# Optimization experiments

Hardware: AMD Instinct MI355X
Metric: run time of the kernel (lower is better)

## Reference

```python
import jax, jax.numpy as jnp
import numpy as np

B, L, HIDDEN, DEPTH, INPUT_DIM = 256, 4096, 128, 2, 2
LOG_PROB_FACTOR = 0.5


def setup_inputs() -> dict:
    key = jax.random.key(0)
    k1, k2, k3, k4 = jax.random.split(key, 4)
    x = jax.random.randint(k1, (B, L), 0, INPUT_DIM)
    # variance-scaling-like init (fan_avg), small scale for recurrent stability
    W_in = jax.random.normal(k2, (INPUT_DIM, HIDDEN), dtype=jnp.float32) * np.float32(
        (2.0 / (INPUT_DIM + HIDDEN)) ** 0.5)
    W_c = jax.random.normal(k3, (DEPTH, HIDDEN, HIDDEN), dtype=jnp.float32) * np.float32(
        (0.1 / HIDDEN) ** 0.5)
    W_out = jax.random.normal(k4, (HIDDEN, INPUT_DIM - 1), dtype=jnp.float32) * np.float32(
        (2.0 / (HIDDEN + INPUT_DIM - 1)) ** 0.5)
    b_out = jnp.zeros((INPUT_DIM - 1,), dtype=jnp.float32)
    return {"x": x, "W_in": W_in, "W_c": W_c, "W_out": W_out, "b_out": b_out}


def reference(x, W_in, W_c, W_out, b_out):
    # x: [B, L] int spins; returns per-sample summed log-prob [B]
    b, l = x.shape
    input_dim = W_in.shape[0]
    depth, hidden = W_c.shape[0], W_c.shape[1]

    oh = jax.nn.one_hot(x, input_dim, dtype=W_in.dtype)       # [B, L, D_in]
    xs = jnp.moveaxis(oh, 1, 0)                                # [L, B, D_in]

    h0 = jnp.zeros((b, depth, hidden), dtype=W_in.dtype)       # zero_carry
    prev0 = jnp.zeros((b, input_dim), dtype=W_in.dtype)        # initial input

    def step(carry, x_t):
        h, prev = carry
        # data_in_dense + actFun (shared across the stack call)
        r = jax.nn.elu(prev @ W_in)                            # [B, H]
        new_h = []
        for j in range(depth):
            # RNNCell: elu(cell_carry_dense(h_j)) + input
            hj = jax.nn.elu(h[:, j] @ W_c[j]) + r              # [B, H]
            new_h.append(hj)
            r = hj
        h_new = jnp.stack(new_h, axis=1)                       # [B, depth, H]
        # output head -> normalized log-probs (realValuedOutput=True)
        logits = r @ W_out + b_out                             # [B, D_in-1]
        amp = jnp.concatenate(
            [jnp.zeros((b, 1), dtype=logits.dtype), logits], axis=-1)  # [B, D_in]
        lp = LOG_PROB_FACTOR * jax.nn.log_softmax(amp, axis=-1)
        log_p = jnp.sum(lp * x_t, axis=-1)                     # [B]
        log_p = jnp.nan_to_num(log_p, nan=-35.0)
        return (h_new, x_t), log_p

    _, log_ps = jax.lax.scan(step, (h0, prev0), xs)            # [L, B]
    return jnp.sum(log_ps, axis=0)                             # [B]
```

## Files before the change

### kernel.cpp

```cpp
#include <hip/hip_runtime.h>
#include <hip/hip_bf16.h>


#define L_LEN 4096
#define HID   128
#define NB    16
#define TPB   512
#define WPITCH 129

typedef float f32x4 __attribute__((ext_vector_type(4)));
typedef short s16x8 __attribute__((ext_vector_type(8)));
typedef short s16x4 __attribute__((ext_vector_type(4)));

__device__ __forceinline__ float eluf(float v) { return v > 0.f ? v : (__expf(v) - 1.f); }
__device__ __forceinline__ unsigned short f2bf(float v) {
    union { __hip_bfloat16 b; unsigned short u; } cv;
    cv.b = __float2bfloat16(v);
    return cv.u;
}
__device__ __forceinline__ float bf2f(unsigned short u) {
    union { float f; unsigned v; } cv;
    cv.v = ((unsigned)u) << 16;
    return cv.f;
}

__global__ __launch_bounds__(TPB, 1)
void rnn_ls_kernel(const int*   __restrict__ x,
                   const float* __restrict__ W_in,
                   const float* __restrict__ W_c,
                   const float* __restrict__ W_out,
                   const float* __restrict__ b_out,
                   float* __restrict__ out)
{
    __shared__ __align__(16) unsigned short hAf[2][2][NB][HID];
    __shared__ unsigned xbsm[NB * WPITCH];
    __shared__ float gbuf[2][4][NB];

    const int T  = threadIdx.x;
    const int w8 = T >> 6;
    const int Lw = w8 >> 2;
    const int wv = w8 & 3;
    const int l  = T & 63, c = l & 15, g = l >> 4;
    const int bb0 = blockIdx.x * NB;
    const int swz = c << 3;

    for (int idx = w8; idx < NB * (L_LEN / 64); idx += 8) {
        int batch = idx >> 6;
        int pos   = ((idx & 63) << 6) + l;
        int v     = x[(bb0 + batch) * L_LEN + pos];
        unsigned long long mask = __ballot(v & 1);
        if (l == 0)  xbsm[batch * WPITCH + ((idx & 63) << 1)]     = (unsigned)mask;
        if (l == 32) xbsm[batch * WPITCH + ((idx & 63) << 1) + 1] = (unsigned)(mask >> 32);
    }
    for (int i = T; i < 2 * 2 * NB * HID; i += TPB) ((unsigned short*)hAf)[i] = 0;

    s16x8 Af[2][4];
    #pragma unroll
    for (int mt = 0; mt < 2; ++mt) {
        const int col = wv * 32 + mt * 16 + c;
        #pragma unroll
        for (int kt = 0; kt < 4; ++kt) {
            s16x8 f;
            #pragma unroll
            for (int j = 0; j < 8; ++j)
                f[j] = (short)f2bf(W_c[(Lw * HID + kt * 32 + g * 8 + j) * HID + col]);
            Af[mt][kt] = f;
        }
    }
    s16x8 woA;
    #pragma unroll
    for (int j = 0; j < 8; ++j)
        woA[j] = (c == 0) ? (short)f2bf(W_out[wv * 32 + g * 8 + j]) : (short)0;

    float R0v[2][4], R1v[2][4];
    #pragma unroll
    for (int mt = 0; mt < 2; ++mt)
      #pragma unroll
      for (int r = 0; r < 4; ++r) {
        int co = wv * 32 + mt * 16 + 4 * g + r;
        R0v[mt][r] = eluf(W_in[co]);
        R1v[mt][r] = eluf(W_in[HID + co]);
      }
    const float b0 = b_out[0];

    const int ro0 = (g * 8) ^ swz,      ro1 = (32 + g * 8) ^ swz;
    const int ro2 = (64 + g * 8) ^ swz, ro3 = (96 + g * 8) ^ swz;
    const int wo0 = (wv * 32 + 4 * g) ^ swz;
    const int wo1 = (wv * 32 + 16 + 4 * g) ^ swz;

    float acc = 0.f;
    unsigned xw = 0;

    __syncthreads();

#define STEP(T_, Q_) do {                                                         \
    const int t_ = (T_);                                                          \
    s16x8 Bv0, Bv1, Bv2, Bv3;                                                     \
    if ((Lw == 1) || (t_ < L_LEN)) {                                              \
        Bv0 = *(const s16x8*)&hAf[Q_][Lw][c][ro0];                                \
        Bv1 = *(const s16x8*)&hAf[Q_][Lw][c][ro1];                                \
        Bv2 = *(const s16x8*)&hAf[Q_][Lw][c][ro2];                                \
        Bv3 = *(const s16x8*)&hAf[Q_][Lw][c][ro3];                                \
    }                                                                             \
    if (Lw == 1) {                   \
        s16x8 Bw = (wv == 0) ? Bv0 : (wv == 1) ? Bv1 : (wv == 2) ? Bv2 : Bv3;     \
        f32x4 Cg = {0.f, 0.f, 0.f, 0.f};                                          \
        Cg = __builtin_amdgcn_mfma_f32_16x16x32_bf16(woA, Bw, Cg, 0, 0, 0);       \
        if (g == 0) gbuf[Q_][wv][c] = Cg[0];                                      \
    }                                                                             \
    if (w8 == 7 && l < 16 && t_ > 1) {                \
        int s_ = t_ - 2;                                                          \
        float gg = gbuf[Q_ ^ 1][0][c] + gbuf[Q_ ^ 1][1][c]                        \
                 + gbuf[Q_ ^ 1][2][c] + gbuf[Q_ ^ 1][3][c] + b0;                  \
        unsigned cw = xbsm[c * WPITCH + (s_ >> 5)];                               \
        int bit = (cw >> (s_ & 31)) & 1;                                          \
        float mm  = fmaxf(gg, 0.f);                                               \
        float lse = mm + __logf(__expf(gg - mm) + __expf(-mm));                   \
        acc += 0.5f * ((bit ? gg : 0.f) - lse);                                   \
    }                                                                             \
    f32x4 CA = {0.f, 0.f, 0.f, 0.f}, CB = {0.f, 0.f, 0.f, 0.f};                   \
    if (t_ < L_LEN) {                                                             \
        CA = __builtin_amdgcn_mfma_f32_16x16x32_bf16(Af[0][0], Bv0, CA, 0, 0, 0); \
        CA = __builtin_amdgcn_mfma_f32_16x16x32_bf16(Af[0][1], Bv1, CA, 0, 0, 0); \
        CA = __builtin_amdgcn_mfma_f32_16x16x32_bf16(Af[0][2], Bv2, CA, 0, 0, 0); \
        CA = __builtin_amdgcn_mfma_f32_16x16x32_bf16(Af[0][3], Bv3, CA, 0, 0, 0); \
        CB = __builtin_amdgcn_mfma_f32_16x16x32_bf16(Af[1][0], Bv0, CB, 0, 0, 0); \
        CB = __builtin_amdgcn_mfma_f32_16x16x32_bf16(Af[1][1], Bv1, CB, 0, 0, 0); \
        CB = __builtin_amdgcn_mfma_f32_16x16x32_bf16(Af[1][2], Bv2, CB, 0, 0, 0); \
        CB = __builtin_amdgcn_mfma_f32_16x16x32_bf16(Af[1][3], Bv3, CB, 0, 0, 0); \
        if (Lw == 0) {                   \
            if (((t_ - 1) & 31) == 0) xw = xbsm[c * WPITCH + ((t_ - 1) >> 5)];    \
            const int bit = (int)((xw >> ((t_ - 1) & 31)) & 1u);                  \
            s16x4 p0, p1;                                                         \
            _Pragma("unroll")                                                     \
            for (int r = 0; r < 4; ++r) {                                         \
                p0[r] = (short)f2bf(eluf(CA[r]) + (bit ? R1v[0][r] : R0v[0][r])); \
                p1[r] = (short)f2bf(eluf(CB[r]) + (bit ? R1v[1][r] : R0v[1][r])); \
            }                                                                     \
            *(s16x4*)&hAf[Q_ ^ 1][0][c][wo0] = p0;                                \
            *(s16x4*)&hAf[Q_ ^ 1][0][c][wo1] = p1;                                \
        }                                                                         \
    }                                                                             \
    __syncthreads();                                                              \
    if (Lw == 1 && t_ < L_LEN) {            \
        s16x4 h0a = *(const s16x4*)&hAf[Q_ ^ 1][0][c][wo0];                       \
        s16x4 h0b = *(const s16x4*)&hAf[Q_ ^ 1][0][c][wo1];                       \
        s16x4 p0, p1;                                                             \
        _Pragma("unroll")                                                         \
        for (int r = 0; r < 4; ++r) {                                             \
            p0[r] = (short)f2bf(eluf(CA[r]) + bf2f((unsigned short)h0a[r]));      \
            p1[r] = (short)f2bf(eluf(CB[r]) + bf2f((unsigned short)h0b[r]));      \
        }                                                                         \
        *(s16x4*)&hAf[Q_ ^ 1][1][c][wo0] = p0;                                    \
        *(s16x4*)&hAf[Q_ ^ 1][1][c][wo1] = p1;                                    \
    }                                                                             \
    __syncthreads();                                                              \
} while (0)

    for (int t = 1; t <= L_LEN; t += 2) {
        STEP(t, 1);
        STEP(t + 1, 0);
    }
#undef STEP

    if (w8 == 7 && l < 16) {
        float gg = gbuf[0][0][c] + gbuf[0][1][c] + gbuf[0][2][c] + gbuf[0][3][c] + b0;
        unsigned cw = xbsm[c * WPITCH + ((L_LEN - 1) >> 5)];
        int bit = (cw >> ((L_LEN - 1) & 31)) & 1;
        float mm  = fmaxf(gg, 0.f);
        float lse = mm + __logf(__expf(gg - mm) + __expf(-mm));
        acc += 0.5f * ((bit ? gg : 0.f) - lse);
        out[bb0 + c] = acc;
    }
}

extern "C" void kernel_launch(void* const* d_in, const int* in_sizes, int n_in,
                              void* d_out, int out_size, void* d_ws, size_t ws_size,
                              hipStream_t stream)
{
    const int*   x     = (const int*)  d_in[0];
    const float* W_in  = (const float*)d_in[1];
    const float* W_c   = (const float*)d_in[2];
    const float* W_out = (const float*)d_in[3];
    const float* b_out = (const float*)d_in[4];
    float* out = (float*)d_out;

    rnn_ls_kernel<<<16, TPB, 0, stream>>>(x, W_in, W_c, W_out, b_out, out);
}
```

Before: 2.756 ms.

## Software-pipeline the two RNN layers across timesteps with one barrier per step

Layer 1 waves now process the previous timestep while layer 0 waves compute the current one, so each step needs a single __syncthreads instead of two. The output-head MFMA and log-softmax are shifted further down the pipeline with a 4-deep gbuf ring, and the loop is extended by extra drain iterations. bf16 packing now uses the v_cvt_pk_bf16_f32 instruction through inline asm. This halves the barrier count on the sequential critical path, in exchange for more complex index bookkeeping and a few extra loop iterations.

```diff
diff --git a/kernel.cpp b/kernel.cpp
--- a/kernel.cpp
+++ b/kernel.cpp
@@ -10,31 +10,32 @@
 
 typedef float f32x4 __attribute__((ext_vector_type(4)));
 typedef short s16x8 __attribute__((ext_vector_type(8)));
-typedef short s16x4 __attribute__((ext_vector_type(4)));
+
+#define MFMA16(A_, B_, C_) __builtin_amdgcn_mfma_f32_16x16x32_bf16((A_), (B_), (C_), 0, 0, 0)
 
 __device__ __forceinline__ float eluf(float v) { return v > 0.f ? v : (__expf(v) - 1.f); }
+__device__ __forceinline__ unsigned cvtpk(float lo, float hi) {
+    unsigned r;
+    asm("v_cvt_pk_bf16_f32 %0, %1, %2" : "=v"(r) : "v"(lo), "v"(hi));
+    return r;
+}
 __device__ __forceinline__ unsigned short f2bf(float v) {
     union { __hip_bfloat16 b; unsigned short u; } cv;
     cv.b = __float2bfloat16(v);
     return cv.u;
 }
-__device__ __forceinline__ float bf2f(unsigned short u) {
-    union { float f; unsigned v; } cv;
-    cv.v = ((unsigned)u) << 16;
-    return cv.f;
-}
 
 __global__ __launch_bounds__(TPB, 1)
-void rnn_ls_kernel(const int*   __restrict__ x,
-                   const float* __restrict__ W_in,
-                   const float* __restrict__ W_c,
-                   const float* __restrict__ W_out,
-                   const float* __restrict__ b_out,
-                   float* __restrict__ out)
+void rnn_pipe_kernel(const int*   __restrict__ x,
+                     const float* __restrict__ W_in,
+                     const float* __restrict__ W_c,
+                     const float* __restrict__ W_out,
+                     const float* __restrict__ b_out,
+                     float* __restrict__ out)
 {
     __shared__ __align__(16) unsigned short hAf[2][2][NB][HID];
     __shared__ unsigned xbsm[NB * WPITCH];
-    __shared__ float gbuf[2][4][NB];
+    __shared__ float gbuf[4][4][NB];
 
     const int T  = threadIdx.x;
     const int w8 = T >> 6;
@@ -85,6 +86,7 @@
 
     const int ro0 = (g * 8) ^ swz,      ro1 = (32 + g * 8) ^ swz;
     const int ro2 = (64 + g * 8) ^ swz, ro3 = (96 + g * 8) ^ swz;
+    const int ro_w = (wv * 32 + g * 8) ^ swz;
     const int wo0 = (wv * 32 + 4 * g) ^ swz;
     const int wo1 = (wv * 32 + 16 + 4 * g) ^ swz;
 
@@ -95,83 +97,93 @@
 
 #define STEP(T_, Q_) do {                                                         \
     const int t_ = (T_);                                                          \
-    s16x8 Bv0, Bv1, Bv2, Bv3;                                                     \
-    if ((Lw == 1) || (t_ < L_LEN)) {                                              \
-        Bv0 = *(const s16x8*)&hAf[Q_][Lw][c][ro0];                                \
-        Bv1 = *(const s16x8*)&hAf[Q_][Lw][c][ro1];                                \
-        Bv2 = *(const s16x8*)&hAf[Q_][Lw][c][ro2];                                \
-        Bv3 = *(const s16x8*)&hAf[Q_][Lw][c][ro3];                                \
-    }                                                                             \
-    if (Lw == 1) {                   \
-        s16x8 Bw = (wv == 0) ? Bv0 : (wv == 1) ? Bv1 : (wv == 2) ? Bv2 : Bv3;     \
-        f32x4 Cg = {0.f, 0.f, 0.f, 0.f};                                          \
-        Cg = __builtin_amdgcn_mfma_f32_16x16x32_bf16(woA, Bw, Cg, 0, 0, 0);       \
-        if (g == 0) gbuf[Q_][wv][c] = Cg[0];                                      \
-    }                                                                             \
-    if (w8 == 7 && l < 16 && t_ > 1) {                \
-        int s_ = t_ - 2;                                                          \
-        float gg = gbuf[Q_ ^ 1][0][c] + gbuf[Q_ ^ 1][1][c]                        \
-                 + gbuf[Q_ ^ 1][2][c] + gbuf[Q_ ^ 1][3][c] + b0;                  \
-        unsigned cw = xbsm[c * WPITCH + (s_ >> 5)];                               \
-        int bit = (cw >> (s_ & 31)) & 1;                                          \
-        float mm  = fmaxf(gg, 0.f);                                               \
-        float lse = mm + __logf(__expf(gg - mm) + __expf(-mm));                   \
-        acc += 0.5f * ((bit ? gg : 0.f) - lse);                                   \
-    }                                                                             \
-    f32x4 CA = {0.f, 0.f, 0.f, 0.f}, CB = {0.f, 0.f, 0.f, 0.f};                   \
-    if (t_ < L_LEN) {                                                             \
-        CA = __builtin_amdgcn_mfma_f32_16x16x32_bf16(Af[0][0], Bv0, CA, 0, 0, 0); \
-        CA = __builtin_amdgcn_mfma_f32_16x16x32_bf16(Af[0][1], Bv1, CA, 0, 0, 0); \
-        CA = __builtin_amdgcn_mfma_f32_16x16x32_bf16(Af[0][2], Bv2, CA, 0, 0, 0); \
-        CA = __builtin_amdgcn_mfma_f32_16x16x32_bf16(Af[0][3], Bv3, CA, 0, 0, 0); \
-        CB = __builtin_amdgcn_mfma_f32_16x16x32_bf16(Af[1][0], Bv0, CB, 0, 0, 0); \
-        CB = __builtin_amdgcn_mfma_f32_16x16x32_bf16(Af[1][1], Bv1, CB, 0, 0, 0); \
-        CB = __builtin_amdgcn_mfma_f32_16x16x32_bf16(Af[1][2], Bv2, CB, 0, 0, 0); \
-        CB = __builtin_amdgcn_mfma_f32_16x16x32_bf16(Af[1][3], Bv3, CB, 0, 0, 0); \
-        if (Lw == 0) {                   \
+    if (Lw == 0) {                                                                \
+        if (t_ < L_LEN) {                                \
+            s16x8 B0 = *(const s16x8*)&hAf[Q_][0][c][ro0];                        \
+            s16x8 B1 = *(const s16x8*)&hAf[Q_][0][c][ro1];                        \
+            s16x8 B2 = *(const s16x8*)&hAf[Q_][0][c][ro2];                        \
+            s16x8 B3 = *(const s16x8*)&hAf[Q_][0][c][ro3];                        \
             if (((t_ - 1) & 31) == 0) xw = xbsm[c * WPITCH + ((t_ - 1) >> 5)];    \
+            f32x4 CA = {0.f,0.f,0.f,0.f}, CB = {0.f,0.f,0.f,0.f};                 \
+            CA = MFMA16(Af[0][0], B0, CA); CA = MFMA16(Af[0][1], B1, CA);         \
+            CA = MFMA16(Af[0][2], B2, CA); CA = MFMA16(Af[0][3], B3, CA);         \
+            CB = MFMA16(Af[1][0], B0, CB); CB = MFMA16(Af[1][1], B1, CB);         \
+            CB = MFMA16(Af[1][2], B2, CB); CB = MFMA16(Af[1][3], B3, CB);         \
             const int bit = (int)((xw >> ((t_ - 1) & 31)) & 1u);                  \
-            s16x4 p0, p1;                                                         \
-            _Pragma("unroll")                                                     \
-            for (int r = 0; r < 4; ++r) {                                         \
-                p0[r] = (short)f2bf(eluf(CA[r]) + (bit ? R1v[0][r] : R0v[0][r])); \
-                p1[r] = (short)f2bf(eluf(CB[r]) + (bit ? R1v[1][r] : R0v[1][r])); \
-            }                                                                     \
-            *(s16x4*)&hAf[Q_ ^ 1][0][c][wo0] = p0;                                \
-            *(s16x4*)&hAf[Q_ ^ 1][0][c][wo1] = p1;                                \
+            float ha0 = eluf(CA[0]) + (bit ? R1v[0][0] : R0v[0][0]);              \
+            float ha1 = eluf(CA[1]) + (bit ? R1v[0][1] : R0v[0][1]);              \
+            float ha2 = eluf(CA[2]) + (bit ? R1v[0][2] : R0v[0][2]);              \
+            float ha3 = eluf(CA[3]) + (bit ? R1v[0][3] : R0v[0][3]);              \
+            float hb0 = eluf(CB[0]) + (bit ? R1v[1][0] : R0v[1][0]);              \
+            float hb1 = eluf(CB[1]) + (bit ? R1v[1][1] : R0v[1][1]);              \
+            float hb2 = eluf(CB[2]) + (bit ? R1v[1][2] : R0v[1][2]);              \
+            float hb3 = eluf(CB[3]) + (bit ? R1v[1][3] : R0v[1][3]);              \
+            uint2 pa, pb;                                                         \
+            pa.x = cvtpk(ha0, ha1); pa.y = cvtpk(ha2, ha3);                       \
+            pb.x = cvtpk(hb0, hb1); pb.y = cvtpk(hb2, hb3);                       \
+            *(uint2*)&hAf[Q_ ^ 1][0][c][wo0] = pa;                                \
+            *(uint2*)&hAf[Q_ ^ 1][0][c][wo1] = pb;                                \
+        }                                                                         \
+    } else {                                                                      \
+        if (t_ >= 2 && t_ <= L_LEN) {                                \
+            s16x8 B0 = *(const s16x8*)&hAf[Q_][1][c][ro0];                        \
+            s16x8 B1 = *(const s16x8*)&hAf[Q_][1][c][ro1];                        \
+            s16x8 B2 = *(const s16x8*)&hAf[Q_][1][c][ro2];                        \
+            s16x8 B3 = *(const s16x8*)&hAf[Q_][1][c][ro3];                        \
+            uint2 a0 = *(const uint2*)&hAf[Q_][0][c][wo0];      \
+            uint2 a1 = *(const uint2*)&hAf[Q_][0][c][wo1];                        \
+            s16x8 Bw = B0;                                                        \
+            if (wv == 1) Bw = B1; else if (wv == 2) Bw = B2;                      \
+            else if (wv == 3) Bw = B3;                                            \
+            f32x4 Cg = {0.f,0.f,0.f,0.f};                                         \
+            Cg = MFMA16(woA, Bw, Cg);          \
+            if (g == 0) gbuf[t_ & 3][wv][c] = Cg[0];                              \
+            f32x4 CA = {0.f,0.f,0.f,0.f}, CB = {0.f,0.f,0.f,0.f};                 \
+            CA = MFMA16(Af[0][0], B0, CA); CA = MFMA16(Af[0][1], B1, CA);         \
+            CA = MFMA16(Af[0][2], B2, CA); CA = MFMA16(Af[0][3], B3, CA);         \
+            CB = MFMA16(Af[1][0], B0, CB); CB = MFMA16(Af[1][1], B1, CB);         \
+            CB = MFMA16(Af[1][2], B2, CB); CB = MFMA16(Af[1][3], B3, CB);         \
+            float ha0 = eluf(CA[0]) + __uint_as_float(a0.x << 16);                \
+            float ha1 = eluf(CA[1]) + __uint_as_float(a0.x & 0xffff0000u);        \
+            float ha2 = eluf(CA[2]) + __uint_as_float(a0.y << 16);                \
+            float ha3 = eluf(CA[3]) + __uint_as_float(a0.y & 0xffff0000u);        \
+            float hb0 = eluf(CB[0]) + __uint_as_float(a1.x << 16);                \
+            float hb1 = eluf(CB[1]) + __uint_as_float(a1.x & 0xffff0000u);        \
+            float hb2 = eluf(CB[2]) + __uint_as_float(a1.y << 16);                \
+            float hb3 = eluf(CB[3]) + __uint_as_float(a1.y & 0xffff0000u);        \
+            uint2 pa, pb;                                                         \
+            pa.x = cvtpk(ha0, ha1); pa.y = cvtpk(ha2, ha3);                       \
+            pb.x = cvtpk(hb0, hb1); pb.y = cvtpk(hb2, hb3);                       \
+            *(uint2*)&hAf[Q_ ^ 1][1][c][wo0] = pa;                                \
+            *(uint2*)&hAf[Q_ ^ 1][1][c][wo1] = pb;                                \
+        } else if (t_ == L_LEN + 1) {                  \
+            s16x8 Bw = *(const s16x8*)&hAf[Q_][1][c][ro_w];                       \
+            f32x4 Cg = {0.f,0.f,0.f,0.f};                                         \
+            Cg = MFMA16(woA, Bw, Cg);                                             \
+            if (g == 0) gbuf[t_ & 3][wv][c] = Cg[0];                              \
+        }                                                                         \
+        if (w8 == 7 && l < 16 && t_ >= 4 && t_ <= L_LEN + 3) {       \
+            int s_ = t_ - 4;                                                      \
+            const float* gp = &gbuf[(t_ - 2) & 3][0][0];                          \
+            float gg = gp[0 * NB + c] + gp[1 * NB + c]                            \
+                     + gp[2 * NB + c] + gp[3 * NB + c] + b0;                      \
+            unsigned cw = xbsm[c * WPITCH + (s_ >> 5)];                           \
+            int bit2 = (cw >> (s_ & 31)) & 1;                                     \
+            float mm  = fmaxf(gg, 0.f);                                           \
+            float lse = mm + __logf(__expf(gg - mm) + __expf(-mm));               \
+            acc += 0.5f * ((bit2 ? gg : 0.f) - lse);                              \
         }                                                                         \
     }                                                                             \
     __syncthreads();                                                              \
-    if (Lw == 1 && t_ < L_LEN) {            \
-        s16x4 h0a = *(const s16x4*)&hAf[Q_ ^ 1][0][c][wo0];                       \
-        s16x4 h0b = *(const s16x4*)&hAf[Q_ ^ 1][0][c][wo1];                       \
-        s16x4 p0, p1;                                                             \
-        _Pragma("unroll")                                                         \
-        for (int r = 0; r < 4; ++r) {                                             \
-            p0[r] = (short)f2bf(eluf(CA[r]) + bf2f((unsigned short)h0a[r]));      \
-            p1[r] = (short)f2bf(eluf(CB[r]) + bf2f((unsigned short)h0b[r]));      \
-        }                                                                         \
-        *(s16x4*)&hAf[Q_ ^ 1][1][c][wo0] = p0;                                    \
-        *(s16x4*)&hAf[Q_ ^ 1][1][c][wo1] = p1;                                    \
-    }                                                                             \
-    __syncthreads();                                                              \
 } while (0)
 
-    for (int t = 1; t <= L_LEN; t += 2) {
+    for (int t = 1; t <= L_LEN + 3; t += 2) {
         STEP(t, 1);
         STEP(t + 1, 0);
     }
 #undef STEP
 
-    if (w8 == 7 && l < 16) {
-        float gg = gbuf[0][0][c] + gbuf[0][1][c] + gbuf[0][2][c] + gbuf[0][3][c] + b0;
-        unsigned cw = xbsm[c * WPITCH + ((L_LEN - 1) >> 5)];
-        int bit = (cw >> ((L_LEN - 1) & 31)) & 1;
-        float mm  = fmaxf(gg, 0.f);
-        float lse = mm + __logf(__expf(gg - mm) + __expf(-mm));
-        acc += 0.5f * ((bit ? gg : 0.f) - lse);
-        out[bb0 + c] = acc;
-    }
+    if (w8 == 7 && l < 16) out[bb0 + c] = acc;
 }
 
 extern "C" void kernel_launch(void* const* d_in, const int* in_sizes, int n_in,
@@ -185,5 +197,5 @@
     const float* b_out = (const float*)d_in[4];
     float* out = (float*)d_out;
 
-    rnn_ls_kernel<<<16, TPB, 0, stream>>>(x, W_in, W_c, W_out, b_out, out);
-}
+    rnn_pipe_kernel<<<16, TPB, 0, stream>>>(x, W_in, W_c, W_out, b_out, out);
+}
```

After: 2.550 ms. -7.5%, faster.

## Replace block barriers with LDS flag-based producer/consumer sync between RNN layers

Applied to the files above, without the earlier changes.

Replaces the two __syncthreads per timestep with per-wave atomic flags in LDS. Layer-0 waves and layer-1 waves now run as a decoupled pipeline over a 4-deep ring of hidden-state buffers, each waiting only on the flags it depends on. The per-step log-prob reduction is spread round-robin over the layer-1 waves instead of one wave, and bf16 packing uses v_cvt_pk_bf16_f32. The intent is to cut barrier latency on the serial recurrence critical path. In exchange it adds spin-wait polling and memory-ordering subtleties that could cause stalls or races.

```diff
diff --git a/kernel.cpp b/kernel.cpp
--- a/kernel.cpp
+++ b/kernel.cpp
@@ -10,31 +10,54 @@
 
 typedef float f32x4 __attribute__((ext_vector_type(4)));
 typedef short s16x8 __attribute__((ext_vector_type(8)));
-typedef short s16x4 __attribute__((ext_vector_type(4)));
+
+#define MFMA16(A_, B_, C_) __builtin_amdgcn_mfma_f32_16x16x32_bf16((A_), (B_), (C_), 0, 0, 0)
 
 __device__ __forceinline__ float eluf(float v) { return v > 0.f ? v : (__expf(v) - 1.f); }
+__device__ __forceinline__ unsigned cvtpk(float lo, float hi) {
+    unsigned r;
+    asm("v_cvt_pk_bf16_f32 %0, %1, %2" : "=v"(r) : "v"(lo), "v"(hi));
+    return r;
+}
 __device__ __forceinline__ unsigned short f2bf(float v) {
     union { __hip_bfloat16 b; unsigned short u; } cv;
     cv.b = __float2bfloat16(v);
     return cv.u;
 }
-__device__ __forceinline__ float bf2f(unsigned short u) {
-    union { float f; unsigned v; } cv;
-    cv.v = ((unsigned)u) << 16;
-    return cv.f;
+
+__device__ __forceinline__ void wait_ge(int* f, int skip, int target) {
+    if (target <= 0) return;
+    for (;;) {
+        int ok = 1;
+        #pragma unroll
+        for (int i = 0; i < 4; ++i) {
+            if (i == skip) continue;
+            ok &= (__hip_atomic_load(&f[i], __ATOMIC_ACQUIRE,
+                                     __HIP_MEMORY_SCOPE_WORKGROUP) >= target);
+        }
+        if (ok) break;
+        __builtin_amdgcn_s_sleep(1);
+    }
+    __builtin_amdgcn_sched_barrier(0);
+}
+__device__ __forceinline__ void post(int* f, int v) {
+    asm volatile("s_waitcnt lgkmcnt(0)" ::: "memory");
+    __hip_atomic_store(f, v, __ATOMIC_RELEASE, __HIP_MEMORY_SCOPE_WORKGROUP);
 }
 
 __global__ __launch_bounds__(TPB, 1)
-void rnn_ls_kernel(const int*   __restrict__ x,
-                   const float* __restrict__ W_in,
-                   const float* __restrict__ W_c,
-                   const float* __restrict__ W_out,
-                   const float* __restrict__ b_out,
-                   float* __restrict__ out)
+void rnn_async_kernel(const int*   __restrict__ x,
+                      const float* __restrict__ W_in,
+                      const float* __restrict__ W_c,
+                      const float* __restrict__ W_out,
+                      const float* __restrict__ b_out,
+                      float* __restrict__ out)
 {
-    __shared__ __align__(16) unsigned short hAf[2][2][NB][HID];
+    __shared__ __align__(16) unsigned short hAf[4][2][NB][HID];
     __shared__ unsigned xbsm[NB * WPITCH];
-    __shared__ float gbuf[2][4][NB];
+    __shared__ float gbuf[4][4][NB];
+    __shared__ float accb[4][NB];
+    __shared__ int flag0[4], flag1[4];
 
     const int T  = threadIdx.x;
     const int w8 = T >> 6;
@@ -52,7 +75,8 @@
         if (l == 0)  xbsm[batch * WPITCH + ((idx & 63) << 1)]     = (unsigned)mask;
         if (l == 32) xbsm[batch * WPITCH + ((idx & 63) << 1) + 1] = (unsigned)(mask >> 32);
     }
-    for (int i = T; i < 2 * 2 * NB * HID; i += TPB) ((unsigned short*)hAf)[i] = 0;
+    for (int i = T; i < 4 * 2 * NB * HID; i += TPB) ((unsigned short*)hAf)[i] = 0;
+    if (T < 4) { flag0[T] = 0; flag1[T] = 0; }
 
     s16x8 Af[2][4];
     #pragma unroll
@@ -88,89 +112,118 @@
     const int wo0 = (wv * 32 + 4 * g) ^ swz;
     const int wo1 = (wv * 32 + 16 + 4 * g) ^ swz;
 
-    float acc = 0.f;
-    unsigned xw = 0;
-
     __syncthreads();
 
-#define STEP(T_, Q_) do {                                                         \
-    const int t_ = (T_);                                                          \
-    s16x8 Bv0, Bv1, Bv2, Bv3;                                                     \
-    if ((Lw == 1) || (t_ < L_LEN)) {                                              \
-        Bv0 = *(const s16x8*)&hAf[Q_][Lw][c][ro0];                                \
-        Bv1 = *(const s16x8*)&hAf[Q_][Lw][c][ro1];                                \
-        Bv2 = *(const s16x8*)&hAf[Q_][Lw][c][ro2];                                \
-        Bv3 = *(const s16x8*)&hAf[Q_][Lw][c][ro3];                                \
-    }                                                                             \
-    if (Lw == 1) {                   \
-        s16x8 Bw = (wv == 0) ? Bv0 : (wv == 1) ? Bv1 : (wv == 2) ? Bv2 : Bv3;     \
-        f32x4 Cg = {0.f, 0.f, 0.f, 0.f};                                          \
-        Cg = __builtin_amdgcn_mfma_f32_16x16x32_bf16(woA, Bw, Cg, 0, 0, 0);       \
-        if (g == 0) gbuf[Q_][wv][c] = Cg[0];                                      \
-    }                                                                             \
-    if (w8 == 7 && l < 16 && t_ > 1) {                \
-        int s_ = t_ - 2;                                                          \
-        float gg = gbuf[Q_ ^ 1][0][c] + gbuf[Q_ ^ 1][1][c]                        \
-                 + gbuf[Q_ ^ 1][2][c] + gbuf[Q_ ^ 1][3][c] + b0;                  \
-        unsigned cw = xbsm[c * WPITCH + (s_ >> 5)];                               \
-        int bit = (cw >> (s_ & 31)) & 1;                                          \
-        float mm  = fmaxf(gg, 0.f);                                               \
-        float lse = mm + __logf(__expf(gg - mm) + __expf(-mm));                   \
-        acc += 0.5f * ((bit ? gg : 0.f) - lse);                                   \
-    }                                                                             \
-    f32x4 CA = {0.f, 0.f, 0.f, 0.f}, CB = {0.f, 0.f, 0.f, 0.f};                   \
-    if (t_ < L_LEN) {                                                             \
-        CA = __builtin_amdgcn_mfma_f32_16x16x32_bf16(Af[0][0], Bv0, CA, 0, 0, 0); \
-        CA = __builtin_amdgcn_mfma_f32_16x16x32_bf16(Af[0][1], Bv1, CA, 0, 0, 0); \
-        CA = __builtin_amdgcn_mfma_f32_16x16x32_bf16(Af[0][2], Bv2, CA, 0, 0, 0); \
-        CA = __builtin_amdgcn_mfma_f32_16x16x32_bf16(Af[0][3], Bv3, CA, 0, 0, 0); \
-        CB = __builtin_amdgcn_mfma_f32_16x16x32_bf16(Af[1][0], Bv0, CB, 0, 0, 0); \
-        CB = __builtin_amdgcn_mfma_f32_16x16x32_bf16(Af[1][1], Bv1, CB, 0, 0, 0); \
-        CB = __builtin_amdgcn_mfma_f32_16x16x32_bf16(Af[1][2], Bv2, CB, 0, 0, 0); \
-        CB = __builtin_amdgcn_mfma_f32_16x16x32_bf16(Af[1][3], Bv3, CB, 0, 0, 0); \
-        if (Lw == 0) {                   \
-            if (((t_ - 1) & 31) == 0) xw = xbsm[c * WPITCH + ((t_ - 1) >> 5)];    \
-            const int bit = (int)((xw >> ((t_ - 1) & 31)) & 1u);                  \
-            s16x4 p0, p1;                                                         \
-            _Pragma("unroll")                                                     \
-            for (int r = 0; r < 4; ++r) {                                         \
-                p0[r] = (short)f2bf(eluf(CA[r]) + (bit ? R1v[0][r] : R0v[0][r])); \
-                p1[r] = (short)f2bf(eluf(CB[r]) + (bit ? R1v[1][r] : R0v[1][r])); \
-            }                                                                     \
-            *(s16x4*)&hAf[Q_ ^ 1][0][c][wo0] = p0;                                \
-            *(s16x4*)&hAf[Q_ ^ 1][0][c][wo1] = p1;                                \
-        }                                                                         \
-    }                                                                             \
-    __syncthreads();                                                              \
-    if (Lw == 1 && t_ < L_LEN) {            \
-        s16x4 h0a = *(const s16x4*)&hAf[Q_ ^ 1][0][c][wo0];                       \
-        s16x4 h0b = *(const s16x4*)&hAf[Q_ ^ 1][0][c][wo1];                       \
-        s16x4 p0, p1;                                                             \
-        _Pragma("unroll")                                                         \
-        for (int r = 0; r < 4; ++r) {                                             \
-            p0[r] = (short)f2bf(eluf(CA[r]) + bf2f((unsigned short)h0a[r]));      \
-            p1[r] = (short)f2bf(eluf(CB[r]) + bf2f((unsigned short)h0b[r]));      \
-        }                                                                         \
-        *(s16x4*)&hAf[Q_ ^ 1][1][c][wo0] = p0;                                    \
-        *(s16x4*)&hAf[Q_ ^ 1][1][c][wo1] = p1;                                    \
-    }                                                                             \
-    __syncthreads();                                                              \
-} while (0)
-
-    for (int t = 1; t <= L_LEN; t += 2) {
-        STEP(t, 1);
-        STEP(t + 1, 0);
-    }
-#undef STEP
-
-    if (w8 == 7 && l < 16) {
-        float gg = gbuf[0][0][c] + gbuf[0][1][c] + gbuf[0][2][c] + gbuf[0][3][c] + b0;
-        unsigned cw = xbsm[c * WPITCH + ((L_LEN - 1) >> 5)];
-        int bit = (cw >> ((L_LEN - 1) & 31)) & 1;
-        float mm  = fmaxf(gg, 0.f);
-        float lse = mm + __logf(__expf(gg - mm) + __expf(-mm));
-        acc += 0.5f * ((bit ? gg : 0.f) - lse);
-        out[bb0 + c] = acc;
+    if (Lw == 0) {
+        unsigned xw = 0;
+        for (int t = 1; t < L_LEN; ++t) {
+            wait_ge(flag0, wv, t - 1);
+            wait_ge(flag1, -1, t - 3);
+
+            const unsigned short* hp = &hAf[(t - 1) & 3][0][c][0];
+            s16x8 B0 = *(const s16x8*)&hp[ro0];
+            s16x8 B1 = *(const s16x8*)&hp[ro1];
+            s16x8 B2 = *(const s16x8*)&hp[ro2];
+            s16x8 B3 = *(const s16x8*)&hp[ro3];
+            if (((t - 1) & 31) == 0) xw = xbsm[c * WPITCH + ((t - 1) >> 5)];
+
+            f32x4 CA = {0.f,0.f,0.f,0.f}, CB = {0.f,0.f,0.f,0.f};
+            CA = MFMA16(Af[0][0], B0, CA); CA = MFMA16(Af[0][1], B1, CA);
+            CA = MFMA16(Af[0][2], B2, CA); CA = MFMA16(Af[0][3], B3, CA);
+            CB = MFMA16(Af[1][0], B0, CB); CB = MFMA16(Af[1][1], B1, CB);
+            CB = MFMA16(Af[1][2], B2, CB); CB = MFMA16(Af[1][3], B3, CB);
+
+            const int bit = (int)((xw >> ((t - 1) & 31)) & 1u);
+            float ha0 = eluf(CA[0]) + (bit ? R1v[0][0] : R0v[0][0]);
+            float ha1 = eluf(CA[1]) + (bit ? R1v[0][1] : R0v[0][1]);
+            float ha2 = eluf(CA[2]) + (bit ? R1v[0][2] : R0v[0][2]);
+            float ha3 = eluf(CA[3]) + (bit ? R1v[0][3] : R0v[0][3]);
+            float hb0 = eluf(CB[0]) + (bit ? R1v[1][0] : R0v[1][0]);
+            float hb1 = eluf(CB[1]) + (bit ? R1v[1][1] : R0v[1][1]);
+            float hb2 = eluf(CB[2]) + (bit ? R1v[1][2] : R0v[1][2]);
+            float hb3 = eluf(CB[3]) + (bit ? R1v[1][3] : R0v[1][3]);
+            uint2 pa, pb;
+            pa.x = cvtpk(ha0, ha1); pa.y = cvtpk(ha2, ha3);
+            pb.x = cvtpk(hb0, hb1); pb.y = cvtpk(hb2, hb3);
+            *(uint2*)&hAf[t & 3][0][c][wo0] = pa;
+            *(uint2*)&hAf[t & 3][0][c][wo1] = pb;
+
+            post(&flag0[wv], t);
+        }
+    } else {
+        float acc = 0.f;
+        for (int u = 1; u <= L_LEN; ++u) {
+            wait_ge(flag1, wv, u - 1);
+            wait_ge(flag0, -1, u < L_LEN ? u : L_LEN - 1);
+
+            const unsigned short* hp = &hAf[(u - 1) & 3][1][c][0];
+            s16x8 B0 = *(const s16x8*)&hp[ro0];
+            s16x8 B1 = *(const s16x8*)&hp[ro1];
+            s16x8 B2 = *(const s16x8*)&hp[ro2];
+            s16x8 B3 = *(const s16x8*)&hp[ro3];
+
+            {
+                s16x8 Bw = B0;
+                if (wv == 1) Bw = B1; else if (wv == 2) Bw = B2;
+                else if (wv == 3) Bw = B3;
+                f32x4 Cg = {0.f,0.f,0.f,0.f};
+                Cg = MFMA16(woA, Bw, Cg);
+                if (g == 0) gbuf[(u - 1) & 3][wv][c] = Cg[0];
+            }
+
+            if (u < L_LEN) {
+                uint2 a0 = *(const uint2*)&hAf[u & 3][0][c][wo0];
+                uint2 a1 = *(const uint2*)&hAf[u & 3][0][c][wo1];
+                f32x4 CA = {0.f,0.f,0.f,0.f}, CB = {0.f,0.f,0.f,0.f};
+                CA = MFMA16(Af[0][0], B0, CA); CA = MFMA16(Af[0][1], B1, CA);
+                CA = MFMA16(Af[0][2], B2, CA); CA = MFMA16(Af[0][3], B3, CA);
+                CB = MFMA16(Af[1][0], B0, CB); CB = MFMA16(Af[1][1], B1, CB);
+                CB = MFMA16(Af[1][2], B2, CB); CB = MFMA16(Af[1][3], B3, CB);
+                float ha0 = eluf(CA[0]) + __uint_as_float(a0.x << 16);
+                float ha1 = eluf(CA[1]) + __uint_as_float(a0.x & 0xffff0000u);
+                float ha2 = eluf(CA[2]) + __uint_as_float(a0.y << 16);
+                float ha3 = eluf(CA[3]) + __uint_as_float(a0.y & 0xffff0000u);
+                float hb0 = eluf(CB[0]) + __uint_as_float(a1.x << 16);
+                float hb1 = eluf(CB[1]) + __uint_as_float(a1.x & 0xffff0000u);
+                float hb2 = eluf(CB[2]) + __uint_as_float(a1.y << 16);
+                float hb3 = eluf(CB[3]) + __uint_as_float(a1.y & 0xffff0000u);
+                uint2 pa, pb;
+                pa.x = cvtpk(ha0, ha1); pa.y = cvtpk(ha2, ha3);
+                pb.x = cvtpk(hb0, hb1); pb.y = cvtpk(hb2, hb3);
+                *(uint2*)&hAf[u & 3][1][c][wo0] = pa;
+                *(uint2*)&hAf[u & 3][1][c][wo1] = pb;
+            }
+
+            post(&flag1[wv], u);
+
+            int s_ = u - 2;
+            if (s_ >= 0 && ((s_ & 3) == wv) && l < 16) {
+                float gg = gbuf[s_ & 3][0][c] + gbuf[s_ & 3][1][c]
+                         + gbuf[s_ & 3][2][c] + gbuf[s_ & 3][3][c] + b0;
+                unsigned cw = xbsm[c * WPITCH + (s_ >> 5)];
+                int bit = (cw >> (s_ & 31)) & 1;
+                float mm  = fmaxf(gg, 0.f);
+                float lse = mm + __logf(__expf(gg - mm) + __expf(-mm));
+                acc += 0.5f * ((bit ? gg : 0.f) - lse);
+            }
+        }
+        if (l < 16) accb[wv][c] = acc;
+        post(&flag1[wv], L_LEN + 1);
+
+        if (w8 == 7) {
+            wait_ge(flag1, -1, L_LEN + 1);
+            if (l < 16) {
+                float gg = gbuf[3][0][c] + gbuf[3][1][c]
+                         + gbuf[3][2][c] + gbuf[3][3][c] + b0;
+                unsigned cw = xbsm[c * WPITCH + ((L_LEN - 1) >> 5)];
+                int bit = (cw >> ((L_LEN - 1) & 31)) & 1;
+                float mm  = fmaxf(gg, 0.f);
+                float lse = mm + __logf(__expf(gg - mm) + __expf(-mm));
+                float tail = 0.5f * ((bit ? gg : 0.f) - lse);
+                out[bb0 + c] = accb[0][c] + accb[1][c] + accb[2][c]
+                             + accb[3][c] + tail;
+            }
+        }
     }
 }
 
@@ -185,5 +238,5 @@
     const float* b_out = (const float*)d_in[4];
     float* out = (float*)d_out;
 
-    rnn_ls_kernel<<<16, TPB, 0, stream>>>(x, W_in, W_c, W_out, b_out, out);
-}
+    rnn_async_kernel<<<16, TPB, 0, stream>>>(x, W_in, W_c, W_out, b_out, out);
+}
```

New measurement: 3.412 ms. 1.24x slower.
